# Kernel optimization log

Hardware: AMD Instinct MI355X
Metric: run time of the kernel (lower is better)

Reference implementation:

```python
import jax, jax.numpy as jnp
import numpy as np


def setup_inputs() -> dict:
    key = jax.random.key(0)
    k1, k2 = jax.random.split(key)
    N, C, H, W = 4, 128, 160, 320
    left = jax.random.normal(k1, (N, C, H, W), dtype=jnp.float32)
    right = jax.random.normal(k2, (N, C, H, W), dtype=jnp.float32)
    return {"left": left, "right": right, "max_disparity": 48}


def reference(left, right, max_disparity):
    # left, right: (N, C, H, W) -> volume: (N, D, H, W)
    # volume[n, d, h, w] = sum_c left[n, c, h, w] * right[n, c, h, w - d]  (0 if w < d)
    n, c, h, w = left.shape
    slices = []
    for d in range(max_disparity):  # fixed structural constant, unrolled at trace time
        # channel dot-product of overlapping strips, shape (N, H, W - d)
        corr = jnp.einsum('nchw,nchw->nhw', left[:, :, :, d:], right[:, :, :, :w - d])
        # left-pad the first d columns with zeros to restore width W
        slices.append(jnp.pad(corr, ((0, 0), (0, 0), (d, 0))))
    return jnp.stack(slices, axis=1)  # (N, D, H, W)
```

## Files before the change

kernel.cpp:

```cpp
#include <hip/hip_runtime.h>


#define NN 4
#define CC 128
#define HH 160
#define WW 320
#define DD 48
#define HWs (HH * WW)
#define WB 160
#define RJ 208

typedef _Float16 h2 __attribute__((ext_vector_type(2)));
typedef __fp16 h2raw __attribute__((ext_vector_type(2)));

union V4 { float4 f; h2 h[4]; };

__device__ __forceinline__ h2 pack2(float a, float b) {
  union { h2raw r; h2 h; } u;
  u.r = __builtin_amdgcn_cvt_pkrtz(a, b);
  return u.h;
}

__device__ __forceinline__ float dot2(h2 a, h2 b, float c) {
  return __builtin_amdgcn_fdot2(a, b, c, false);
}

__global__ __launch_bounds__(256, 5)
void corr_kernel(const float* __restrict__ L, const float* __restrict__ R,
                 float* __restrict__ out) {
  __shared__ __align__(16) h2 Lsp[2][8][WB];
  __shared__ __align__(16) h2 Rsp[2][8][RJ];

  const int tid = threadIdx.x;
  const int wg = tid & 31;
  const int jg = tid >> 5;
  const int bid = blockIdx.x;
  const int wsplit = bid & 1;
  const int row = bid >> 1;
  const int n = row / HH;
  const int h = row - n * HH;
  const int wb = wsplit * WB;

  const int u0 = 5 * wg;
  int S = (u0 + 1) & ~7;
  if (S > RJ - 64) S = RJ - 64;
  const int js0 = S + 8 * jg;

  const size_t base = (size_t)n * CC * HWs + (size_t)h * WW;
  const float* Lb = L + base + wb;
  const float* Rb = R + base + (wb - 48);

  float acc[5][8];
#pragma unroll
  for (int i = 0; i < 5; ++i)
#pragma unroll
    for (int k = 0; k < 8; ++k) acc[i][k] = 0.f;

  auto stage = [&](int q, int b) {
    const int c0 = 16 * q;
    for (int t = tid; t < 320; t += 256) {
      const int cp = t / 40, v = t - cp * 40;
      const float* p = Lb + (size_t)(c0 + 2 * cp) * HWs + 4 * v;
      const float4 a = *(const float4*)p;
      const float4 c = *(const float4*)(p + HWs);
      V4 u;
      u.h[0] = pack2(a.x, c.x); u.h[1] = pack2(a.y, c.y);
      u.h[2] = pack2(a.z, c.z); u.h[3] = pack2(a.w, c.w);
      *(float4*)&Lsp[b][cp][4 * v] = u.f;
    }
    for (int t = tid; t < 416; t += 256) {
      const int cp = t / 52, v = t - cp * 52;
      float4 a = {0.f, 0.f, 0.f, 0.f}, c = {0.f, 0.f, 0.f, 0.f};
      if (wb - 48 + 4 * v >= 0) {
        const float* p = Rb + (size_t)(c0 + 2 * cp) * HWs + 4 * v;
        a = *(const float4*)p;
        c = *(const float4*)(p + HWs);
      }
      V4 u;
      u.h[0] = pack2(a.x, c.x); u.h[1] = pack2(a.y, c.y);
      u.h[2] = pack2(a.z, c.z); u.h[3] = pack2(a.w, c.w);
      *(float4*)&Rsp[b][cp][4 * v] = u.f;
    }
  };

  auto compute = [&](int b) {
#pragma unroll
    for (int cpl = 0; cpl < 8; ++cpl) {
      h2 lv[5];
#pragma unroll
      for (int i = 0; i < 5; ++i) lv[i] = Lsp[b][cpl][u0 + i];
      V4 r0, r1;
      r0.f = *(const float4*)&Rsp[b][cpl][js0];
      r1.f = *(const float4*)&Rsp[b][cpl][js0 + 4];
      h2 rv[8] = {r0.h[0], r0.h[1], r0.h[2], r0.h[3],
                  r1.h[0], r1.h[1], r1.h[2], r1.h[3]};
#pragma unroll
      for (int i = 0; i < 5; ++i)
#pragma unroll
        for (int k = 0; k < 8; ++k)
          acc[i][k] = dot2(lv[i], rv[k], acc[i][k]);
    }
  };

  stage(0, 0);
  __syncthreads();
  for (int q = 0; q < 8; ++q) {
    const int b = q & 1;
    if (q < 7) stage(q + 1, b ^ 1);
    compute(b);
    __syncthreads();
  }

  float* ob = out + (size_t)n * DD * HWs + (size_t)h * WW + wb + u0;
#pragma unroll
  for (int i = 0; i < 5; ++i)
#pragma unroll
    for (int k = 0; k < 8; ++k) {
      const int d = u0 + i + 48 - (js0 + k);
      if (d >= 0 && d < DD) ob[(size_t)d * HWs + i] = acc[i][k];
    }
}

extern "C" void kernel_launch(void* const* d_in, const int* in_sizes, int n_in,
                              void* d_out, int out_size, void* d_ws, size_t ws_size,
                              hipStream_t stream) {
  const float* L = (const float*)d_in[0];
  const float* R = (const float*)d_in[1];
  float* out = (float*)d_out;
  corr_kernel<<<dim3(2 * NN * HH), dim3(256), 0, stream>>>(L, R, out);
}
```

Before: 277.5 us.

## Rewrite correlation as banded MFMA f16 matmul with swizzled LDS and staged stores

Replaces the fdot2-based scalar accumulation with 16x16x32 f16 MFMA instructions, computing banded tiles of the left-right channel product. The kernel now uses 640 threads per block. All 128 channels of the right strip are loaded in one pass into a single XOR-swizzled LDS buffer, and the left values are held in registers instead of the double-buffered per-channel staging loop. Output goes through an LDS epilogue so each disparity row is written with coalesced float4 stores. This aims to cut ALU instruction count and non-coalesced scattered global writes, at the cost of a large block, more registers, and no overlap between loading and compute.

```diff
diff --git a/kernel.cpp b/kernel.cpp
--- a/kernel.cpp
+++ b/kernel.cpp
@@ -8,12 +8,14 @@
 #define DD 48
 #define HWs (HH * WW)
 #define WB 160
-#define RJ 208
+#define RROWS 208
+#define RPITCH 68
+#define RTASKS 3328
 
 typedef _Float16 h2 __attribute__((ext_vector_type(2)));
+typedef _Float16 f16x8 __attribute__((ext_vector_type(8)));
+typedef float f32x4 __attribute__((ext_vector_type(4)));
 typedef __fp16 h2raw __attribute__((ext_vector_type(2)));
-
-union V4 { float4 f; h2 h[4]; };
 
 __device__ __forceinline__ h2 pack2(float a, float b) {
   union { h2raw r; h2 h; } u;
@@ -21,104 +23,108 @@
   return u.h;
 }
 
-__device__ __forceinline__ float dot2(h2 a, h2 b, float c) {
-  return __builtin_amdgcn_fdot2(a, b, c, false);
-}
-
-__global__ __launch_bounds__(256, 5)
+__global__ __launch_bounds__(640)
 void corr_kernel(const float* __restrict__ L, const float* __restrict__ R,
                  float* __restrict__ out) {
-  __shared__ __align__(16) h2 Lsp[2][8][WB];
-  __shared__ __align__(16) h2 Rsp[2][8][RJ];
+  __shared__ __align__(16) h2 Rh[RROWS][RPITCH];
 
   const int tid = threadIdx.x;
-  const int wg = tid & 31;
-  const int jg = tid >> 5;
+  const int wt  = tid >> 6;
+  const int ln  = tid & 63;
+  const int i16 = ln & 15;
+  const int g   = ln >> 4;
+
   const int bid = blockIdx.x;
   const int wsplit = bid & 1;
-  const int row = bid >> 1;
-  const int n = row / HH;
-  const int h = row - n * HH;
+  const int row_nh = bid >> 1;
+  const int n = row_nh / HH;
+  const int h = row_nh - n * HH;
   const int wb = wsplit * WB;
 
-  const int u0 = 5 * wg;
-  int S = (u0 + 1) & ~7;
-  if (S > RJ - 64) S = RJ - 64;
-  const int js0 = S + 8 * jg;
+  const size_t base = (size_t)n * CC * HWs + (size_t)h * WW;
+  const float* Rbase = R + base;
+  const float* Lbase = L + base + wb + 16 * wt + i16;
 
-  const size_t base = (size_t)n * CC * HWs + (size_t)h * WW;
-  const float* Lb = L + base + wb;
-  const float* Rb = R + base + (wb - 48);
-
-  float acc[5][8];
+  union F4 { float4 f; float a[4]; };
+  F4 ra[6], rc[6];
 #pragma unroll
-  for (int i = 0; i < 5; ++i)
-#pragma unroll
-    for (int k = 0; k < 8; ++k) acc[i][k] = 0.f;
-
-  auto stage = [&](int q, int b) {
-    const int c0 = 16 * q;
-    for (int t = tid; t < 320; t += 256) {
-      const int cp = t / 40, v = t - cp * 40;
-      const float* p = Lb + (size_t)(c0 + 2 * cp) * HWs + 4 * v;
-      const float4 a = *(const float4*)p;
-      const float4 c = *(const float4*)(p + HWs);
-      V4 u;
-      u.h[0] = pack2(a.x, c.x); u.h[1] = pack2(a.y, c.y);
-      u.h[2] = pack2(a.z, c.z); u.h[3] = pack2(a.w, c.w);
-      *(float4*)&Lsp[b][cp][4 * v] = u.f;
+  for (int it = 0; it < 6; ++it) {
+    int t = tid + it * 640;
+    ra[it].f = make_float4(0.f, 0.f, 0.f, 0.f);
+    rc[it].f = make_float4(0.f, 0.f, 0.f, 0.f);
+    if (t < RTASKS) {
+      int c2 = t / 52, v = t - 52 * c2;
+      int col = wb - 48 + 4 * v;
+      if (col >= 0) {
+        const float* p = Rbase + (size_t)(2 * c2) * HWs + col;
+        ra[it].f = *(const float4*)p;
+        rc[it].f = *(const float4*)(p + HWs);
+      }
     }
-    for (int t = tid; t < 416; t += 256) {
-      const int cp = t / 52, v = t - cp * 52;
-      float4 a = {0.f, 0.f, 0.f, 0.f}, c = {0.f, 0.f, 0.f, 0.f};
-      if (wb - 48 + 4 * v >= 0) {
-        const float* p = Rb + (size_t)(c0 + 2 * cp) * HWs + 4 * v;
-        a = *(const float4*)p;
-        c = *(const float4*)(p + HWs);
-      }
-      V4 u;
-      u.h[0] = pack2(a.x, c.x); u.h[1] = pack2(a.y, c.y);
-      u.h[2] = pack2(a.z, c.z); u.h[3] = pack2(a.w, c.w);
-      *(float4*)&Rsp[b][cp][4 * v] = u.f;
-    }
-  };
-
-  auto compute = [&](int b) {
-#pragma unroll
-    for (int cpl = 0; cpl < 8; ++cpl) {
-      h2 lv[5];
-#pragma unroll
-      for (int i = 0; i < 5; ++i) lv[i] = Lsp[b][cpl][u0 + i];
-      V4 r0, r1;
-      r0.f = *(const float4*)&Rsp[b][cpl][js0];
-      r1.f = *(const float4*)&Rsp[b][cpl][js0 + 4];
-      h2 rv[8] = {r0.h[0], r0.h[1], r0.h[2], r0.h[3],
-                  r1.h[0], r1.h[1], r1.h[2], r1.h[3]};
-#pragma unroll
-      for (int i = 0; i < 5; ++i)
-#pragma unroll
-        for (int k = 0; k < 8; ++k)
-          acc[i][k] = dot2(lv[i], rv[k], acc[i][k]);
-    }
-  };
-
-  stage(0, 0);
-  __syncthreads();
-  for (int q = 0; q < 8; ++q) {
-    const int b = q & 1;
-    if (q < 7) stage(q + 1, b ^ 1);
-    compute(b);
-    __syncthreads();
   }
 
-  float* ob = out + (size_t)n * DD * HWs + (size_t)h * WW + wb + u0;
+  float lv[32];
 #pragma unroll
-  for (int i = 0; i < 5; ++i)
+  for (int ks = 0; ks < 4; ++ks)
 #pragma unroll
-    for (int k = 0; k < 8; ++k) {
-      const int d = u0 + i + 48 - (js0 + k);
-      if (d >= 0 && d < DD) ob[(size_t)d * HWs + i] = acc[i][k];
+    for (int e = 0; e < 8; ++e)
+      lv[ks * 8 + e] = Lbase[(size_t)(32 * ks + 8 * g + e) * HWs];
+
+#pragma unroll
+  for (int it = 0; it < 6; ++it) {
+    int t = tid + it * 640;
+    if (t < RTASKS) {
+      int c2 = t / 52, v = t - 52 * c2;
+      int colp = c2 ^ (4 * (v & 7));
+#pragma unroll
+      for (int i = 0; i < 4; ++i)
+        Rh[4 * v + i][colp] = pack2(ra[it].a[i], rc[it].a[i]);
     }
+  }
+
+  union AU { f16x8 v; h2 h[4]; };
+  AU A[4];
+#pragma unroll
+  for (int ks = 0; ks < 4; ++ks)
+#pragma unroll
+    for (int j = 0; j < 4; ++j)
+      A[ks].h[j] = pack2(lv[ks * 8 + 2 * j], lv[ks * 8 + 2 * j + 1]);
+
+  __syncthreads();
+
+  f32x4 acc[4] = {};
+#pragma unroll
+  for (int q = 0; q < 4; ++q) {
+    const int row = 16 * (wt + q) + i16;
+    const int swz = 4 * ((row >> 2) & 7);
+    union BU { float4 f; f16x8 v; } B;
+#pragma unroll
+    for (int ks = 0; ks < 4; ++ks) {
+      B.f = *(const float4*)&Rh[row][(16 * ks + 4 * g) ^ swz];
+      acc[q] = __builtin_amdgcn_mfma_f32_16x16x32_f16(A[ks].v, B.v, acc[q], 0, 0, 0);
+    }
+  }
+
+  __syncthreads();
+
+  float* Ep = ((float*)&Rh[0][0]) + wt * (DD * 20);
+#pragma unroll
+  for (int q = 0; q < 4; ++q)
+#pragma unroll
+    for (int r = 0; r < 4; ++r) {
+      int d = 48 - 16 * q + 4 * g + r - i16;
+      if (d >= 0 && d < DD) Ep[d * 20 + 4 * g + r] = acc[q][r];
+    }
+
+  const int l4 = ln & 3;
+  const int dr = ln >> 2;
+  float* outp = out + (size_t)n * DD * HWs + (size_t)h * WW + wb + 16 * wt + 4 * l4;
+#pragma unroll
+  for (int rr = 0; rr < 3; ++rr) {
+    int d = 16 * rr + dr;
+    float4 val = *(const float4*)&Ep[d * 20 + 4 * l4];
+    *(float4*)&outp[(size_t)d * HWs] = val;
+  }
 }
 
 extern "C" void kernel_launch(void* const* d_in, const int* in_sizes, int n_in,
@@ -127,5 +133,5 @@
   const float* L = (const float*)d_in[0];
   const float* R = (const float*)d_in[1];
   float* out = (float*)d_out;
-  corr_kernel<<<dim3(2 * NN * HH), dim3(256), 0, stream>>>(L, R, out);
+  corr_kernel<<<dim3(2 * NN * HH), dim3(640), 0, stream>>>(L, R, out);
 }
```

Result: faster. 236.1 us (-14.9%).
